# Performance work log

Hardware: AMD Instinct MI355X
Metric: run time of the kernel (lower is better)

Reference implementation:

```python
import jax, jax.numpy as jnp
import numpy as np

B, N, E, H = 4, 2048, 1024, 16
Dh = E // H  # 64


def _rope_tables(n, dh, dtype=jnp.float32):
    inv_freq = 1.0 / (10000.0 ** (jnp.arange(0, dh, 2, dtype=jnp.float32) / dh))
    t = jnp.arange(n, dtype=jnp.float32)
    freqs = jnp.outer(t, inv_freq)            # (N, Dh/2)
    emb = jnp.concatenate([freqs, freqs], -1)  # (N, Dh)
    return jnp.cos(emb).astype(dtype), jnp.sin(emb).astype(dtype)


def _rotate_half(x):
    half = x.shape[-1] // 2
    return jnp.concatenate([-x[..., half:], x[..., :half]], axis=-1)


def _apply_rope(x, cos, sin):
    # x: (B, H, N, Dh); cos/sin: (N, Dh)
    return x * cos[None, None] + _rotate_half(x) * sin[None, None]


def setup_inputs() -> dict:
    key = jax.random.key(0)
    ks = jax.random.split(key, 10)
    x = jax.random.normal(ks[0], (B, N, E), dtype=jnp.float32)
    s = 0.02
    wq = jax.random.normal(ks[1], (E, E), jnp.float32) * s
    bq = jnp.zeros((E,), jnp.float32)
    wk = jax.random.normal(ks[2], (E, E), jnp.float32) * s
    bk = jnp.zeros((E,), jnp.float32)
    wv = jax.random.normal(ks[3], (E, E), jnp.float32) * s
    bv = jnp.zeros((E,), jnp.float32)
    wo = jax.random.normal(ks[4], (E, E), jnp.float32) * s
    bo = jnp.zeros((E,), jnp.float32)
    # no padding (all keys valid); flip some entries True to exercise masking if desired
    key_padding_mask = jnp.zeros((B, N), dtype=bool)
    return dict(x=x, wq=wq, bq=bq, wk=wk, bk=bk, wv=wv, bv=bv,
                wo=wo, bo=bo, key_padding_mask=key_padding_mask)


def reference(x, wq, bq, wk, bk, wv, bv, wo, bo, key_padding_mask):
    b, n, e = x.shape

    def proj(w, bvec):
        y = jnp.einsum('bne,fe->bnf', x, w) + bvec  # Linear: x @ W^T + b
        return y.reshape(b, n, H, Dh).transpose(0, 2, 1, 3)  # (B,H,N,Dh)

    Q, K, V = proj(wq, bq), proj(wk, bk), proj(wv, bv)
    cos, sin = _rope_tables(n, Dh, x.dtype)
    Q = _apply_rope(Q, cos, sin)
    K = _apply_rope(K, cos, sin)

    scale = Dh ** -0.5
    attn = jnp.einsum('bhqd,bhkd->bhqk', Q, K) * scale  # (B,H,N,N)
    attn = jnp.where(key_padding_mask[:, None, None, :], -jnp.inf, attn)
    attn = jax.nn.softmax(attn, axis=-1)
    out = jnp.einsum('bhqk,bhkd->bhqd', attn, V)
    out = out.transpose(0, 2, 1, 3).reshape(b, n, e)
    return jnp.einsum('bne,fe->bnf', out, wo) + bo
```

## Files before the change

### kernel.cpp

```cpp
#include <hip/hip_runtime.h>
#include <hip/hip_bf16.h>
#include <stdint.h>

#define B_   4
#define N_   2048
#define E_   1024
#define H_   16
#define DH_  64
#define M_   (B_*N_)
#define KD_  1024

typedef __bf16 bf16x8 __attribute__((ext_vector_type(8)));
typedef float  f32x4  __attribute__((ext_vector_type(4)));
typedef float  f32x16 __attribute__((ext_vector_type(16)));

__device__ __forceinline__ ushort f2bf(float f) {
  union { float f; uint32_t u; } x; x.f = f;
  uint32_t r = x.u + 0x7fffu + ((x.u >> 16) & 1u);
  return (ushort)(r >> 16);
}

__device__ __forceinline__ f32x4 mfma16(bf16x8 a, bf16x8 b, f32x4 c) {
  return __builtin_amdgcn_mfma_f32_16x16x32_bf16(a, b, c, 0, 0, 0);
}
__device__ __forceinline__ f32x16 mfma32(bf16x8 a, bf16x8 b, f32x16 c) {
  return __builtin_amdgcn_mfma_f32_32x32x16_bf16(a, b, c, 0, 0, 0);
}

__device__ __forceinline__ uint32_t cvtpk(float lo, float hi) {
  uint32_t d;
  asm("v_cvt_pk_bf16_f32 %0, %1, %2" : "=v"(d) : "v"(lo), "v"(hi));
  return d;
}

#if __has_builtin(__builtin_amdgcn_exp2f)
#define FEXP2(x) __builtin_amdgcn_exp2f(x)
#else
#define FEXP2(x) exp2f(x)
#endif

__device__ __forceinline__ void gload16(const void* g, void* l) {
  __builtin_amdgcn_global_load_lds(
      (const __attribute__((address_space(1))) uint32_t*)g,
      (__attribute__((address_space(3))) uint32_t*)l, 16, 0, 0);
}

__global__ void cvtk(const float* __restrict__ in, ushort* __restrict__ out, int n) {
  int i = (blockIdx.x * 256 + threadIdx.x) * 4;
  if (i >= n) return;
  float4 v = *(const float4*)(in + i);
  ushort4 o; o.x = f2bf(v.x); o.y = f2bf(v.y); o.z = f2bf(v.z); o.w = f2bf(v.w);
  *(ushort4*)(out + i) = o;
}

__global__ void cvtw(const float* __restrict__ wq, const float* __restrict__ wk,
                     const float* __restrict__ wv, const float* __restrict__ wo,
                     ushort* __restrict__ wqkv, ushort* __restrict__ wob) {
  int i = (blockIdx.x * 256 + threadIdx.x) * 4;
  int which = i >> 20;
  int off = i & 1048575;
  const float* src = which == 0 ? wq : which == 1 ? wk : which == 2 ? wv : wo;
  float4 v = *(const float4*)(src + off);
  ushort4 o; o.x = f2bf(v.x); o.y = f2bf(v.y); o.z = f2bf(v.z); o.w = f2bf(v.w);
  if (which < 3) *(ushort4*)(wqkv + i) = o;
  else           *(ushort4*)(wob + off) = o;
}

__global__ void rope_tables(float* __restrict__ ct, float* __restrict__ st) {
  int idx = blockIdx.x * 256 + threadIdx.x;
  int n = idx >> 5, i = idx & 31;
  double inv = exp(-(double)i * (9.210340371976184 / 32.0));
  float ang = (float)n * (float)inv;
  ct[idx] = cosf(ang);
  st[idx] = sinf(ang);
}

#define GEMM_KLOOP(Aptr, Wptr)                                                 \
  for (int k0 = 0; k0 < KD_; k0 += 64) {                                       \
    _Pragma("unroll")                                                          \
    for (int i = 0; i < 4; ++i) {                                              \
      uint32_t flat = i * 4096 + w * 1024 + lane * 16;                         \
      uint32_t row = flat >> 7, cb = flat & 127;                               \
      uint32_t cbs = cb ^ ((row & 7) << 4);                                    \
      gload16((const char*)(Aptr) + (size_t)(m0 + row) * 2048 + k0 * 2 + cbs,  \
              smA + i * 4096 + w * 1024);                                      \
      gload16((const char*)(Wptr) + (size_t)(n0 + row) * 2048 + k0 * 2 + cbs,  \
              smB + i * 4096 + w * 1024);                                      \
    }                                                                          \
    __syncthreads();                                                           \
    bf16x8 af[4][2], bfr[4][2];                                                \
    _Pragma("unroll")                                                          \
    for (int mf = 0; mf < 4; ++mf)                                             \
      _Pragma("unroll")                                                        \
      for (int kk = 0; kk < 2; ++kk) {                                         \
        int row = wr * 64 + mf * 16 + c;                                       \
        int cb = (kk * 64 + g * 16) ^ ((row & 7) << 4);                        \
        af[mf][kk] = *(const bf16x8*)(smA + row * 128 + cb);                   \
        int rowb = wc * 64 + mf * 16 + c;                                      \
        int cbb = (kk * 64 + g * 16) ^ ((rowb & 7) << 4);                      \
        bfr[mf][kk] = *(const bf16x8*)(smB + rowb * 128 + cbb);                \
      }                                                                        \
    _Pragma("unroll")                                                          \
    for (int kk = 0; kk < 2; ++kk)                                             \
      _Pragma("unroll")                                                        \
      for (int mf = 0; mf < 4; ++mf)                                           \
        _Pragma("unroll")                                                      \
        for (int nf = 0; nf < 4; ++nf)                                         \
          acc[mf][nf] = mfma16(af[mf][kk], bfr[nf][kk], acc[mf][nf]);          \
    __syncthreads();                                                           \
  }

__launch_bounds__(256, 2)
__global__ void gemm_qkv(const ushort* __restrict__ A, const ushort* __restrict__ W,
                         const float* __restrict__ bq, const float* __restrict__ bk,
                         const float* __restrict__ bv,
                         ushort* __restrict__ Qo, ushort* __restrict__ Ko,
                         ushort* __restrict__ Vto,
                         const float* __restrict__ cost, const float* __restrict__ sint)
{
  __shared__ char smem[32768];
  char* smA = smem;
  char* smB = smem + 16384;
  const int tid = threadIdx.x;
  const int lane = tid & 63, w = tid >> 6;
  const int c = lane & 15, g = lane >> 4;
  const int m0 = blockIdx.x * 128, n0 = blockIdx.y * 128;
  const int wr = w >> 1, wc = w & 1;

  f32x4 acc[4][4] = {};
  GEMM_KLOOP(A, W)

  const int sel = n0 >> 10;
  const int ncol = n0 & 1023;
  const int colbase = ncol + wc * 64;
  const int h = colbase >> 6;

  if (sel == 2) {
#pragma unroll
    for (int mf = 0; mf < 4; ++mf) {
      int tok = m0 + wr * 64 + mf * 16 + 4 * g;
      int b = tok >> 11, n = tok & 2047;
#pragma unroll
      for (int nf = 0; nf < 4; ++nf) {
        int d = nf * 16 + c;
        float bvv = bv[colbase + nf * 16 + c];
        ushort4 o;
        o.x = f2bf(acc[mf][nf][0] + bvv);
        o.y = f2bf(acc[mf][nf][1] + bvv);
        o.z = f2bf(acc[mf][nf][2] + bvv);
        o.w = f2bf(acc[mf][nf][3] + bvv);
        *(ushort4*)(Vto + (((size_t)(b * 16 + h) * 64 + d) << 11) + n) = o;
      }
    }
  } else {
    const float* bias = sel ? bk : bq;
    ushort* outB = sel ? Ko : Qo;
    const float sc = sel ? 1.0f : 0.125f * 1.44269504088896340736f;
#pragma unroll
    for (int mf = 0; mf < 4; ++mf) {
#pragma unroll
      for (int r = 0; r < 4; ++r) {
        int tok = m0 + wr * 64 + mf * 16 + 4 * g + r;
        int b = tok >> 11, n = tok & 2047;
        float v[4];
#pragma unroll
        for (int nf = 0; nf < 4; ++nf)
          v[nf] = acc[mf][nf][r] + bias[colbase + nf * 16 + c];
        ushort* orow = outB + ((size_t)(b * 16 + h) * 2048 + n) * 64;
#pragma unroll
        for (int nf = 0; nf < 2; ++nf) {
          int d = nf * 16 + c;
          float cv = cost[n * 32 + d];
          float sv = sint[n * 32 + d];
          orow[d]      = f2bf((v[nf] * cv - v[nf + 2] * sv) * sc);
          orow[d + 32] = f2bf((v[nf + 2] * cv + v[nf] * sv) * sc);
        }
      }
    }
  }
}

__launch_bounds__(256, 2)
__global__ void gemm_out(const ushort* __restrict__ A, const ushort* __restrict__ W,
                         const float* __restrict__ bias, float* __restrict__ outF)
{
  __shared__ char smem[32768];
  char* smA = smem;
  char* smB = smem + 16384;
  const int tid = threadIdx.x;
  const int lane = tid & 63, w = tid >> 6;
  const int c = lane & 15, g = lane >> 4;
  const int m0 = blockIdx.x * 128, n0 = blockIdx.y * 128;
  const int wr = w >> 1, wc = w & 1;

  f32x4 acc[4][4] = {};
  GEMM_KLOOP(A, W)

  const int colbase = n0 + wc * 64;
#pragma unroll
  for (int mf = 0; mf < 4; ++mf) {
    int rowb = m0 + wr * 64 + mf * 16 + 4 * g;
#pragma unroll
    for (int nf = 0; nf < 4; ++nf) {
      int f = colbase + nf * 16 + c;
      float bvv = bias[f];
#pragma unroll
      for (int r = 0; r < 4; ++r)
        outF[(size_t)(rowb + r) * 1024 + f] = acc[mf][nf][r] + bvv;
    }
  }
}

__launch_bounds__(512, 4)
__global__ void flash_k(const ushort* __restrict__ Q, const ushort* __restrict__ K,
                        const ushort* __restrict__ Vt, const uint8_t* __restrict__ mask,
                        ushort* __restrict__ O)
{
  __shared__ char smem[36864];
  const int tid = threadIdx.x;
  const int lane = tid & 63, w = tid >> 6;
  const int l31 = lane & 31, hi = lane >> 5;
  const int q0 = blockIdx.x * 256;
  const int h = blockIdx.y, b = blockIdx.z;
  const size_t head = (size_t)(b * 16 + h) * (2048 * 64);
  const ushort* Qh = Q + head;
  const uint8_t* mb = mask + b * 2048;

  const int qrow = q0 + w * 32 + l31;
  bf16x8 qf[4];
#pragma unroll
  for (int kk = 0; kk < 4; ++kk)
    qf[kk] = *(const bf16x8*)(Qh + (size_t)qrow * 64 + kk * 16 + hi * 8);

  uint64_t mm;
  {
    const uint64_t* m64 = (const uint64_t*)mb;
    mm = m64[lane * 4 + 0] | m64[lane * 4 + 1] | m64[lane * 4 + 2] | m64[lane * 4 + 3];
  }
  const bool anymask = __any(mm != 0);

  bf16x8 vones;
#pragma unroll
  for (int j = 0; j < 8; ++j) vones[j] = (__bf16)1.0f;

  f32x16 Oa0 = {}, Oa1 = {}, Sacc = {};

  const int srow = tid >> 3;
  const int scb = (tid & 7) * 16;
  const int cbs = scb ^ ((srow & 7) << 4);
  const char* Kg = (const char*)(K + head) + srow * 128 + cbs;
  const char* Vg = (const char*)(Vt + head) + srow * 4096 + cbs;

  gload16(Kg, smem + w * 1024);
  gload16(Vg, smem + 8192 + w * 1024);
  Kg += 8192;
  Vg += 128;
  __syncthreads();

  const int swz = (l31 & 7) << 4;

#define FLASH_TILE(T, CBUF, SBUF, DO_STAGE)                                    \
  {                                                                            \
    if (DO_STAGE) {                                                            \
      gload16(Kg, smem + (SBUF) + w * 1024);                                   \
      gload16(Vg, smem + (SBUF) + 8192 + w * 1024);                            \
      Kg += 8192; Vg += 128;                                                   \
    }                                                                          \
    const char* bK = smem + (CBUF);                                            \
    const char* bV = smem + (CBUF) + 8192;                                     \
    f32x16 s0 = {}, s1 = {};                                                   \
    __builtin_amdgcn_s_setprio(1);                                             \
    _Pragma("unroll")                                                          \
    for (int kk = 0; kk < 4; ++kk) {                                           \
      int col = (32 * kk + 16 * hi) ^ swz;                                     \
      bf16x8 k0 = *(const bf16x8*)(bK + l31 * 128 + col);                      \
      bf16x8 k1 = *(const bf16x8*)(bK + (l31 + 32) * 128 + col);               \
      s0 = mfma32(k0, qf[kk], s0);                                             \
      s1 = mfma32(k1, qf[kk], s1);                                             \
    }                                                                          \
    __builtin_amdgcn_s_setprio(0);                                             \
    float p0[16], p1[16];                                                      \
    _Pragma("unroll")                                                          \
    for (int i = 0; i < 16; ++i) {                                             \
      p0[i] = FEXP2(s0[i]);                                                    \
      p1[i] = FEXP2(s1[i]);                                                    \
    }                                                                          \
    if (anymask) {                                                             \
      int kv0 = (T) * 64;                                                      \
      _Pragma("unroll")                                                        \
      for (int r = 0; r < 16; ++r) {                                           \
        int crow = (r & 3) + 8 * (r >> 2) + 4 * hi;                            \
        if (mb[kv0 + crow]) p0[r] = 0.f;                                       \
        if (mb[kv0 + 32 + crow]) p1[r] = 0.f;                                  \
      }                                                                        \
    }                                                                          \
    uint32_t pw[4][4];                                                         \
    _Pragma("unroll")                                                          \
    for (int half = 0; half < 2; ++half) {                                     \
      const float* p = half ? p1 : p0;                                         \
      uint32_t alo0 = cvtpk(p[0], p[1]),  ahi0 = cvtpk(p[2], p[3]);            \
      uint32_t alo1 = cvtpk(p[4], p[5]),  ahi1 = cvtpk(p[6], p[7]);            \
      uint32_t alo2 = cvtpk(p[8], p[9]),  ahi2 = cvtpk(p[10], p[11]);          \
      uint32_t alo3 = cvtpk(p[12], p[13]), ahi3 = cvtpk(p[14], p[15]);         \
      auto r0 = __builtin_amdgcn_permlane32_swap(alo0, alo1, false, false);    \
      auto r1 = __builtin_amdgcn_permlane32_swap(ahi0, ahi1, false, false);    \
      auto r2 = __builtin_amdgcn_permlane32_swap(alo2, alo3, false, false);    \
      auto r3 = __builtin_amdgcn_permlane32_swap(ahi2, ahi3, false, false);    \
      pw[half * 2 + 0][0] = r0[0]; pw[half * 2 + 0][2] = r0[1];                \
      pw[half * 2 + 0][1] = r1[0]; pw[half * 2 + 0][3] = r1[1];                \
      pw[half * 2 + 1][0] = r2[0]; pw[half * 2 + 1][2] = r2[1];                \
      pw[half * 2 + 1][1] = r3[0]; pw[half * 2 + 1][3] = r3[1];                \
    }                                                                          \
    __builtin_amdgcn_s_setprio(1);                                             \
    _Pragma("unroll")                                                          \
    for (int c4 = 0; c4 < 4; ++c4) {                                           \
      union { uint32_t u[4]; bf16x8 v; } pf;                                   \
      pf.u[0] = pw[c4][0]; pf.u[1] = pw[c4][1];                                \
      pf.u[2] = pw[c4][2]; pf.u[3] = pw[c4][3];                                \
      int col = (32 * c4 + 16 * hi) ^ swz;                                     \
      bf16x8 v0 = *(const bf16x8*)(bV + l31 * 128 + col);                      \
      bf16x8 v1 = *(const bf16x8*)(bV + (l31 + 32) * 128 + col);               \
      Oa0 = mfma32(v0, pf.v, Oa0);                                             \
      Oa1 = mfma32(v1, pf.v, Oa1);                                             \
      Sacc = mfma32(vones, pf.v, Sacc);                                        \
    }                                                                          \
    __builtin_amdgcn_s_setprio(0);                                             \
    __syncthreads();                                                           \
  }

  for (int t = 0; t < N_ / 64; t += 2) {
    FLASH_TILE(t,     0,     16384, true)
    FLASH_TILE(t + 1, 16384, 0,     (t + 2 < N_ / 64))
  }
#undef FLASH_TILE

  float inv = 1.0f / Sacc[0];
  char* tr = smem + w * 4608;
#pragma unroll
  for (int db = 0; db < 2; ++db) {
    const f32x16& o = db ? Oa1 : Oa0;
#pragma unroll
    for (int a = 0; a < 4; ++a) {
      uint32_t lo = cvtpk(o[4 * a] * inv, o[4 * a + 1] * inv);
      uint32_t hi2 = cvtpk(o[4 * a + 2] * inv, o[4 * a + 3] * inv);
      *(uint2*)(tr + l31 * 144 + db * 64 + a * 16 + hi * 8) = make_uint2(lo, hi2);
    }
  }
  __asm__ volatile("" ::: "memory");
#pragma unroll
  for (int it = 0; it < 4; ++it) {
    uint4 v = *(const uint4*)(tr + l31 * 144 + it * 32 + hi * 16);
    int n = q0 + w * 32 + l31;
    *(uint4*)(O + (size_t)(b * 2048 + n) * 1024 + h * 64 + it * 16 + hi * 8) = v;
  }
}

extern "C" void kernel_launch(void* const* d_in, const int* in_sizes, int n_in,
                              void* d_out, int out_size, void* d_ws, size_t ws_size,
                              hipStream_t stream)
{
  (void)in_sizes; (void)n_in; (void)out_size; (void)ws_size;
  const float* x  = (const float*)d_in[0];
  const float* wq = (const float*)d_in[1];
  const float* bq = (const float*)d_in[2];
  const float* wk = (const float*)d_in[3];
  const float* bk = (const float*)d_in[4];
  const float* wv = (const float*)d_in[5];
  const float* bv = (const float*)d_in[6];
  const float* wo = (const float*)d_in[7];
  const float* bo = (const float*)d_in[8];
  const uint8_t* mask = (const uint8_t*)d_in[9];
  float* out = (float*)d_out;

  char* ws = (char*)d_ws;
  ushort* xb    = (ushort*)(ws + 0);
  ushort* Ab    = xb;
  ushort* wqkvb = (ushort*)(ws + 16777216);
  ushort* wob   = (ushort*)(ws + 23068672);
  ushort* Qb    = (ushort*)(ws + 25165824);
  ushort* Kb    = (ushort*)(ws + 41943040);
  ushort* Vtb   = (ushort*)(ws + 58720256);
  float*  cost  = (float*)(ws + 75497472);
  float*  sint  = (float*)(ws + 75759616);

  cvtk<<<M_ * KD_ / 4 / 256, 256, 0, stream>>>(x, xb, M_ * KD_);
  cvtw<<<4096, 256, 0, stream>>>(wq, wk, wv, wo, wqkvb, wob);
  rope_tables<<<256, 256, 0, stream>>>(cost, sint);

  gemm_qkv<<<dim3(M_ / 128, 24), 256, 0, stream>>>(xb, wqkvb, bq, bk, bv,
                                                   Qb, Kb, Vtb, cost, sint);

  flash_k<<<dim3(N_ / 256, H_, B_), 512, 0, stream>>>(Qb, Kb, Vtb, mask, Ab);

  gemm_out<<<dim3(M_ / 128, 8), 256, 0, stream>>>(Ab, wob, bo, out);
}
```

Before: 174.8 us.

## Fuse prep kernels, raise GEMM occupancy, remap flash blocks to XCDs

Merges the three preprocessing kernels (x cast, weight cast, rope tables) into one launch to cut launch overhead and the gaps between kernels. Raises the minimum blocks per CU in launch_bounds for both GEMMs from 2 to 3, which may force register limits and spills. Flattens the flash attention grid and remaps block IDs so that the 8 query blocks of a head land on the same XCD, aiming for better L2 reuse of K/V.

```diff
diff --git a/kernel.cpp b/kernel.cpp
--- a/kernel.cpp
+++ b/kernel.cpp
@@ -45,34 +45,36 @@
       (__attribute__((address_space(3))) uint32_t*)l, 16, 0, 0);
 }
 
-__global__ void cvtk(const float* __restrict__ in, ushort* __restrict__ out, int n) {
-  int i = (blockIdx.x * 256 + threadIdx.x) * 4;
-  if (i >= n) return;
-  float4 v = *(const float4*)(in + i);
-  ushort4 o; o.x = f2bf(v.x); o.y = f2bf(v.y); o.z = f2bf(v.z); o.w = f2bf(v.w);
-  *(ushort4*)(out + i) = o;
-}
-
-__global__ void cvtw(const float* __restrict__ wq, const float* __restrict__ wk,
+__global__ void prep(const float* __restrict__ x,
+                     const float* __restrict__ wq, const float* __restrict__ wk,
                      const float* __restrict__ wv, const float* __restrict__ wo,
-                     ushort* __restrict__ wqkv, ushort* __restrict__ wob) {
-  int i = (blockIdx.x * 256 + threadIdx.x) * 4;
-  int which = i >> 20;
-  int off = i & 1048575;
-  const float* src = which == 0 ? wq : which == 1 ? wk : which == 2 ? wv : wo;
-  float4 v = *(const float4*)(src + off);
-  ushort4 o; o.x = f2bf(v.x); o.y = f2bf(v.y); o.z = f2bf(v.z); o.w = f2bf(v.w);
-  if (which < 3) *(ushort4*)(wqkv + i) = o;
-  else           *(ushort4*)(wob + off) = o;
-}
-
-__global__ void rope_tables(float* __restrict__ ct, float* __restrict__ st) {
-  int idx = blockIdx.x * 256 + threadIdx.x;
-  int n = idx >> 5, i = idx & 31;
-  double inv = exp(-(double)i * (9.210340371976184 / 32.0));
-  float ang = (float)n * (float)inv;
-  ct[idx] = cosf(ang);
-  st[idx] = sinf(ang);
+                     ushort* __restrict__ xb, ushort* __restrict__ wqkv,
+                     ushort* __restrict__ wob,
+                     float* __restrict__ ct, float* __restrict__ st)
+{
+  int bid = blockIdx.x;
+  if (bid < 8192) {
+    int i = (bid * 256 + threadIdx.x) * 4;
+    float4 v = *(const float4*)(x + i);
+    ushort4 o; o.x = f2bf(v.x); o.y = f2bf(v.y); o.z = f2bf(v.z); o.w = f2bf(v.w);
+    *(ushort4*)(xb + i) = o;
+  } else if (bid < 12288) {
+    int i = ((bid - 8192) * 256 + threadIdx.x) * 4;
+    int which = i >> 20;
+    int off = i & 1048575;
+    const float* src = which == 0 ? wq : which == 1 ? wk : which == 2 ? wv : wo;
+    float4 v = *(const float4*)(src + off);
+    ushort4 o; o.x = f2bf(v.x); o.y = f2bf(v.y); o.z = f2bf(v.z); o.w = f2bf(v.w);
+    if (which < 3) *(ushort4*)(wqkv + i) = o;
+    else           *(ushort4*)(wob + off) = o;
+  } else {
+    int idx = (bid - 12288) * 256 + threadIdx.x;
+    int n = idx >> 5, i = idx & 31;
+    double inv = exp(-(double)i * (9.210340371976184 / 32.0));
+    float ang = (float)n * (float)inv;
+    ct[idx] = cosf(ang);
+    st[idx] = sinf(ang);
+  }
 }
 
 #define GEMM_KLOOP(Aptr, Wptr)                                                 \
@@ -110,7 +112,7 @@
     __syncthreads();                                                           \
   }
 
-__launch_bounds__(256, 2)
+__launch_bounds__(256, 3)
 __global__ void gemm_qkv(const ushort* __restrict__ A, const ushort* __restrict__ W,
                          const float* __restrict__ bq, const float* __restrict__ bk,
                          const float* __restrict__ bv,
@@ -180,7 +182,7 @@
   }
 }
 
-__launch_bounds__(256, 2)
+__launch_bounds__(256, 3)
 __global__ void gemm_out(const ushort* __restrict__ A, const ushort* __restrict__ W,
                          const float* __restrict__ bias, float* __restrict__ outF)
 {
@@ -220,8 +222,11 @@
   const int tid = threadIdx.x;
   const int lane = tid & 63, w = tid >> 6;
   const int l31 = lane & 31, hi = lane >> 5;
-  const int q0 = blockIdx.x * 256;
-  const int h = blockIdx.y, b = blockIdx.z;
+  const int L = blockIdx.x;
+  const int xcd = L & 7, slot = L >> 3;
+  const int cc = slot >> 3, qb = slot & 7;
+  const int b = cc >> 1, h = xcd + 8 * (cc & 1);
+  const int q0 = qb * 256;
   const size_t head = (size_t)(b * 16 + h) * (2048 * 64);
   const ushort* Qh = Q + head;
   const uint8_t* mb = mask + b * 2048;
@@ -383,14 +388,12 @@
   float*  cost  = (float*)(ws + 75497472);
   float*  sint  = (float*)(ws + 75759616);
 
-  cvtk<<<M_ * KD_ / 4 / 256, 256, 0, stream>>>(x, xb, M_ * KD_);
-  cvtw<<<4096, 256, 0, stream>>>(wq, wk, wv, wo, wqkvb, wob);
-  rope_tables<<<256, 256, 0, stream>>>(cost, sint);
+  prep<<<12544, 256, 0, stream>>>(x, wq, wk, wv, wo, xb, wqkvb, wob, cost, sint);
 
   gemm_qkv<<<dim3(M_ / 128, 24), 256, 0, stream>>>(xb, wqkvb, bq, bk, bv,
                                                    Qb, Kb, Vtb, cost, sint);
 
-  flash_k<<<dim3(N_ / 256, H_, B_), 512, 0, stream>>>(Qb, Kb, Vtb, mask, Ab);
+  flash_k<<<512, 512, 0, stream>>>(Qb, Kb, Vtb, mask, Ab);
 
   gemm_out<<<dim3(M_ / 128, 8), 256, 0, stream>>>(Ab, wob, bo, out);
 }
```

After: 167.2 us (median of 3 runs). 4.4% less time.
